# Kernel optimization log

Measured on AMD Instinct MI355X. Metric: run time of the kernel, lower is better.

The kernel has to match this reference:

```python
import jax, jax.numpy as jnp
import numpy as np

B, T, S, H, L = 64, 512, 400, 768, 9


def setup_inputs() -> dict:
    rng = np.random.default_rng(0)
    attn = np.zeros((B, T), np.int32)
    ids_lens = np.zeros((B, S), np.int32)
    for bi in range(B):
        Lb = int(rng.integers(T // 2, T + 1))  # valid wordpiece count
        lens = []
        rem = Lb
        while rem > 0 and len(lens) < S - 1:
            l = int(min(rng.integers(1, 4), rem))  # 1-3 wordpieces per word
            lens.append(l)
            rem -= l
        if rem > 0:
            lens.append(rem)
        attn[bi, :Lb] = 1
        ids_lens[bi, :len(lens)] = np.asarray(lens, np.int32)
    label_ids = rng.integers(0, L, (B, S)).astype(np.int32)
    label_mask = ids_lens > 0
    key = jax.random.key(0)
    k1, k2 = jax.random.split(key)
    last_enc_out = jax.random.normal(k1, (B, T, H), jnp.float32)
    W = jax.random.normal(k2, (H, L), jnp.float32) * 0.02
    b = jnp.zeros((L,), jnp.float32)
    return {
        'last_enc_out': last_enc_out, 'W': W, 'b': b,
        'attention_mask': jnp.asarray(attn), 'ids_lens': jnp.asarray(ids_lens),
        'label_ids': jnp.asarray(label_ids), 'label_mask': jnp.asarray(label_mask),
    }


def reference(last_enc_out, W, b, attention_mask, ids_lens, label_ids, label_mask):
    Bv, Tv, Hv = last_enc_out.shape
    Sv = ids_lens.shape[1]
    # position of each valid token among the row's valid tokens
    tok_pos = jnp.cumsum(attention_mask, axis=1) - 1            # [B,T]
    cum = jnp.cumsum(ids_lens, axis=1)                          # [B,S] nondecreasing
    # word index for each token: first w with cum[w] > tok_pos
    word_idx = jax.vmap(lambda c, p: jnp.searchsorted(c, p, side='right'))(cum, tok_pos)
    valid = attention_mask > 0
    seg = jnp.where(valid, jnp.arange(Bv)[:, None] * Sv + word_idx, Bv * Sv)  # dump slot for pad
    sums = jax.ops.segment_sum(last_enc_out.reshape(Bv * Tv, Hv), seg.reshape(Bv * Tv),
                               num_segments=Bv * Sv + 1)[:Bv * Sv]
    counts = jnp.maximum(ids_lens.reshape(Bv * Sv), 1).astype(last_enc_out.dtype)
    means = (sums / counts[:, None]).reshape(Bv, Sv, Hv)
    word_mask = ids_lens > 0
    bert_embed = jnp.where(word_mask[:, :, None], means, jnp.zeros((), last_enc_out.dtype))
    # dropout is identity in eval mode
    logits = bert_embed @ W + b                                 # [B,S,L]
    logp = jax.nn.log_softmax(logits, axis=-1)
    nll = -jnp.take_along_axis(logp, label_ids[..., None].astype(jnp.int32), axis=-1)[..., 0]
    mf = label_mask.astype(logits.dtype)
    loss = jnp.sum(nll * mf) / jnp.sum(mf)                      # CE with ignore_index masking
    output = jnp.argmax(logits, axis=-1)
    return loss, output
```

## Files before the change

### kernel.cpp

```cpp
#include <hip/hip_runtime.h>
#include <math.h>

#define Bdim 64
#define Tdim 512
#define Sdim 400
#define Hdim 768
#define Ldim 9

#define QWIN 130
#define LPROJ_ROWS 132

template <int CTRL>
__device__ __forceinline__ float dpp_add(float x) {
  int y = __builtin_amdgcn_update_dpp(0, __float_as_int(x), CTRL, 0xF, 0xF, false);
  return x + __int_as_float(y);
}
__device__ __forceinline__ float wave_sum63(float x) {
  x = dpp_add<0x111>(x);
  x = dpp_add<0x112>(x);
  x = dpp_add<0x114>(x);
  x = dpp_add<0x118>(x);
  x = dpp_add<0x142>(x);
  x = dpp_add<0x143>(x);
  return x;
}

__global__ __launch_bounds__(512, 2) void fused_kernel(
    const float* __restrict__ enc, const float* __restrict__ W,
    const float* __restrict__ bias, const int* __restrict__ attn,
    const int* __restrict__ ids_lens, const int* __restrict__ label_ids,
    float* __restrict__ out, float2* __restrict__ partials) {
  int blk = blockIdx.x;
  int b = blk >> 2;
  int part = blk & 3;
  int q0 = part << 7;
  int tid = threadIdx.x;
  int lane = tid & 63, wid = tid >> 6;

  __shared__ int p2t[Tdim];
  __shared__ int wst[Sdim];
  __shared__ float lproj[LPROJ_ROWS][12];
  __shared__ int wsum[8];
  __shared__ int totsm;
  __shared__ float ssm[8], csm[8];

  int m = attn[b * Tdim + tid];
  int x = m;
#pragma unroll
  for (int off = 1; off < 64; off <<= 1) {
    int v = __shfl_up(x, off, 64);
    if (lane >= off) x += v;
  }
  if (lane == 63) wsum[wid] = x;
  __syncthreads();
  if (tid < 8) {
    int s = wsum[tid], y = s;
#pragma unroll
    for (int off = 1; off < 8; off <<= 1) {
      int v = __shfl_up(y, off, 64);
      if (tid >= off) y += v;
    }
    wsum[tid] = y - s;
    if (tid == 7) totsm = y;
  }
  __syncthreads();
  x += wsum[wid];
  if (m) p2t[x - 1] = tid;
  int nv = totsm;
  __syncthreads();

  int len = (tid < Sdim) ? ids_lens[b * Sdim + tid] : 0;
  int x2 = len;
#pragma unroll
  for (int off = 1; off < 64; off <<= 1) {
    int v = __shfl_up(x2, off, 64);
    if (lane >= off) x2 += v;
  }
  if (lane == 63) wsum[wid] = x2;
  __syncthreads();
  if (tid < 8) {
    int s = wsum[tid], y = s;
#pragma unroll
    for (int off = 1; off < 8; off <<= 1) {
      int v = __shfl_up(y, off, 64);
      if (tid >= off) y += v;
    }
    wsum[tid] = y - s;
  }
  __syncthreads();
  x2 += wsum[wid];
  if (tid < Sdim) wst[tid] = x2 - len;
  __syncthreads();

  int lim = q0 + QWIN;
  if (lim > nv) lim = nv;
  if (wid < 6) {
    int g = (wid >= 3) ? 1 : 0;
    int l0 = (wid - 3 * g) * 3;
    int tc = lim - q0 - g;
    tc = (tc > 0) ? ((tc + 1) >> 1) : 0;

    if (tc > 0) {
      float wf[3][4][3];
#pragma unroll
      for (int k = 0; k < 3; ++k)
#pragma unroll
        for (int j = 0; j < 4; ++j) {
          int h = 4 * lane + 256 * k + j;
#pragma unroll
          for (int c = 0; c < 3; ++c) wf[k][j][c] = W[(size_t)h * Ldim + l0 + c];
        }
      const float4* encb = (const float4*)enc + (size_t)(b << 9) * (Hdim / 4);

      float4 A0, A1, A2, B0, B1, B2;
#define LDK(V0, V1, V2, K)                                                 \
  {                                                                        \
    int t_ = p2t[q0 + g + 2 * (K)];                                        \
    const float4* r_ = encb + (size_t)t_ * (Hdim / 4);                     \
    V0 = r_[lane]; V1 = r_[lane + 64]; V2 = r_[lane + 128];                \
  }
#define PRK(V0, V1, V2, K)                                                 \
  {                                                                        \
    float dd[3];                                                           \
    _Pragma("unroll") for (int c = 0; c < 3; ++c) {                        \
      dd[c] = V0.x * wf[0][0][c] + V0.y * wf[0][1][c] +                    \
              V0.z * wf[0][2][c] + V0.w * wf[0][3][c] +                    \
              V1.x * wf[1][0][c] + V1.y * wf[1][1][c] +                    \
              V1.z * wf[1][2][c] + V1.w * wf[1][3][c] +                    \
              V2.x * wf[2][0][c] + V2.y * wf[2][1][c] +                    \
              V2.z * wf[2][2][c] + V2.w * wf[2][3][c];                     \
      dd[c] = wave_sum63(dd[c]);                                           \
    }                                                                      \
    if (lane == 63) {                                                      \
      int row_ = g + 2 * (K);                                              \
      lproj[row_][l0 + 0] = dd[0];                                         \
      lproj[row_][l0 + 1] = dd[1];                                         \
      lproj[row_][l0 + 2] = dd[2];                                         \
    }                                                                      \
  }
      LDK(A0, A1, A2, 0)
      if (tc > 1) LDK(B0, B1, B2, 1)
      int k = 0;
      for (; k + 2 < tc; k += 2) {
        PRK(A0, A1, A2, k)
        LDK(A0, A1, A2, k + 2)
        PRK(B0, B1, B2, k + 1)
        if (k + 3 < tc) LDK(B0, B1, B2, k + 3)
      }
      PRK(A0, A1, A2, k)
      if (k + 1 < tc) PRK(B0, B1, B2, k + 1)
#undef LDK
#undef PRK
    }
  }
  __syncthreads();

  float nll = 0.0f, cnt = 0.0f;
  if (tid < Sdim) {
    int st = wst[tid];
    int stc = (st > 511) ? 511 : st;
    if ((stc >> 7) == part) {
      int bs = b * Sdim + tid;
      float sum[Ldim];
#pragma unroll
      for (int l = 0; l < Ldim; ++l) sum[l] = 0.0f;
      if (len > 0) {
        for (int j = 0; j < len; ++j) {
          int q = st + j;
          if (q >= nv) break;
          const float* pr = lproj[q - q0];
#pragma unroll
          for (int l = 0; l < Ldim; ++l) sum[l] += pr[l];
        }
      }
      float inv = (len > 0) ? 1.0f / (float)len : 0.0f;
      float lg[Ldim];
#pragma unroll
      for (int l = 0; l < Ldim; ++l) lg[l] = sum[l] * inv + bias[l];

      int amax = 0;
      float mx = lg[0];
#pragma unroll
      for (int l = 1; l < Ldim; ++l)
        if (lg[l] > mx) { mx = lg[l]; amax = l; }
      out[1 + bs] = (float)amax;

      if (len > 0) {
        float se = 0.0f;
#pragma unroll
        for (int l = 0; l < Ldim; ++l) se += expf(lg[l] - mx);
        float lse = mx + logf(se);
        int lab = label_ids[bs];
        float ll = lg[0];
#pragma unroll
        for (int l = 1; l < Ldim; ++l) ll = (lab == l) ? lg[l] : ll;
        nll = lse - ll;
        cnt = 1.0f;
      }
    }
  }

#pragma unroll
  for (int off = 32; off > 0; off >>= 1) {
    nll += __shfl_down(nll, off, 64);
    cnt += __shfl_down(cnt, off, 64);
  }
  if (lane == 0) { ssm[wid] = nll; csm[wid] = cnt; }
  __syncthreads();
  if (tid == 0) {
    float S = 0.f, C = 0.f;
#pragma unroll
    for (int k = 0; k < 8; ++k) { S += ssm[k]; C += csm[k]; }
    float2 pc; pc.x = S; pc.y = C;
    partials[blk] = pc;
  }
}

__global__ __launch_bounds__(256) void final_kernel(
    const float2* __restrict__ partials, float* __restrict__ out) {
  int tid = threadIdx.x;
  float2 pc = partials[tid];
  float s = pc.x, c = pc.y;
#pragma unroll
  for (int off = 32; off > 0; off >>= 1) {
    s += __shfl_down(s, off, 64);
    c += __shfl_down(c, off, 64);
  }
  __shared__ float ss[4], cc[4];
  int wid = tid >> 6, lane = tid & 63;
  if (lane == 0) { ss[wid] = s; cc[wid] = c; }
  __syncthreads();
  if (tid == 0)
    out[0] = (ss[0] + ss[1] + ss[2] + ss[3]) / (cc[0] + cc[1] + cc[2] + cc[3]);
}

extern "C" void kernel_launch(void* const* d_in, const int* in_sizes, int n_in,
                              void* d_out, int out_size, void* d_ws, size_t ws_size,
                              hipStream_t stream) {
  const float* enc     = (const float*)d_in[0];
  const float* W       = (const float*)d_in[1];
  const float* bias    = (const float*)d_in[2];
  const int* attn      = (const int*)d_in[3];
  const int* ids_lens  = (const int*)d_in[4];
  const int* label_ids = (const int*)d_in[5];

  float* out = (float*)d_out;

  float2* partials = (float2*)d_ws;

  fused_kernel<<<Bdim * 4, 512, 0, stream>>>(enc, W, bias, attn, ids_lens,
                                             label_ids, out, partials);
  final_kernel<<<1, 256, 0, stream>>>(partials, out);
}
```

Before: 33.00 us.

## Use all 8 waves for projection with all 9 labels each; fuse final reduction via atomics

New measurement: 36.40 us. +10.3%, slower.

```diff
diff --git a/kernel.cpp b/kernel.cpp
--- a/kernel.cpp
+++ b/kernel.cpp
@@ -25,11 +25,12 @@
   return x;
 }
 
-__global__ __launch_bounds__(512, 2) void fused_kernel(
+__global__ __launch_bounds__(512, 1) void fused_kernel(
     const float* __restrict__ enc, const float* __restrict__ W,
     const float* __restrict__ bias, const int* __restrict__ attn,
     const int* __restrict__ ids_lens, const int* __restrict__ label_ids,
-    float* __restrict__ out, float2* __restrict__ partials) {
+    float* __restrict__ out, float* __restrict__ accum,
+    unsigned* __restrict__ counter) {
   int blk = blockIdx.x;
   int b = blk >> 2;
   int part = blk & 3;
@@ -92,50 +93,46 @@
   if (tid < Sdim) wst[tid] = x2 - len;
   __syncthreads();
 
-  int lim = q0 + QWIN;
-  if (lim > nv) lim = nv;
-  if (wid < 6) {
-    int g = (wid >= 3) ? 1 : 0;
-    int l0 = (wid - 3 * g) * 3;
-    int tc = lim - q0 - g;
-    tc = (tc > 0) ? ((tc + 1) >> 1) : 0;
+  {
+    int lim = q0 + QWIN;
+    if (lim > nv) lim = nv;
+    int tc = lim - q0 - wid;
+    tc = (tc > 0) ? ((tc + 7) >> 3) : 0;
 
     if (tc > 0) {
-      float wf[3][4][3];
-#pragma unroll
-      for (int k = 0; k < 3; ++k)
+      float wf[3][4][Ldim];
+#pragma unroll
+      for (int c = 0; c < 3; ++c)
 #pragma unroll
         for (int j = 0; j < 4; ++j) {
-          int h = 4 * lane + 256 * k + j;
-#pragma unroll
-          for (int c = 0; c < 3; ++c) wf[k][j][c] = W[(size_t)h * Ldim + l0 + c];
+          int h = 4 * lane + 256 * c + j;
+#pragma unroll
+          for (int l = 0; l < Ldim; ++l) wf[c][j][l] = W[(size_t)h * Ldim + l];
         }
       const float4* encb = (const float4*)enc + (size_t)(b << 9) * (Hdim / 4);
 
       float4 A0, A1, A2, B0, B1, B2;
 #define LDK(V0, V1, V2, K)                                                 \
   {                                                                        \
-    int t_ = p2t[q0 + g + 2 * (K)];                                        \
+    int t_ = p2t[q0 + wid + 8 * (K)];                                      \
     const float4* r_ = encb + (size_t)t_ * (Hdim / 4);                     \
     V0 = r_[lane]; V1 = r_[lane + 64]; V2 = r_[lane + 128];                \
   }
 #define PRK(V0, V1, V2, K)                                                 \
   {                                                                        \
-    float dd[3];                                                           \
-    _Pragma("unroll") for (int c = 0; c < 3; ++c) {                        \
-      dd[c] = V0.x * wf[0][0][c] + V0.y * wf[0][1][c] +                    \
-              V0.z * wf[0][2][c] + V0.w * wf[0][3][c] +                    \
-              V1.x * wf[1][0][c] + V1.y * wf[1][1][c] +                    \
-              V1.z * wf[1][2][c] + V1.w * wf[1][3][c] +                    \
-              V2.x * wf[2][0][c] + V2.y * wf[2][1][c] +                    \
-              V2.z * wf[2][2][c] + V2.w * wf[2][3][c];                     \
-      dd[c] = wave_sum63(dd[c]);                                           \
+    float dd[Ldim];                                                        \
+    _Pragma("unroll") for (int l = 0; l < Ldim; ++l) {                     \
+      dd[l] = V0.x * wf[0][0][l] + V0.y * wf[0][1][l] +                    \
+              V0.z * wf[0][2][l] + V0.w * wf[0][3][l] +                    \
+              V1.x * wf[1][0][l] + V1.y * wf[1][1][l] +                    \
+              V1.z * wf[1][2][l] + V1.w * wf[1][3][l] +                    \
+              V2.x * wf[2][0][l] + V2.y * wf[2][1][l] +                    \
+              V2.z * wf[2][2][l] + V2.w * wf[2][3][l];                     \
+      dd[l] = wave_sum63(dd[l]);                                           \
     }                                                                      \
     if (lane == 63) {                                                      \
-      int row_ = g + 2 * (K);                                              \
-      lproj[row_][l0 + 0] = dd[0];                                         \
-      lproj[row_][l0 + 1] = dd[1];                                         \
-      lproj[row_][l0 + 2] = dd[2];                                         \
+      float* dst = lproj[wid + 8 * (K)];                                   \
+      _Pragma("unroll") for (int l = 0; l < Ldim; ++l) dst[l] = dd[l];     \
     }                                                                      \
   }
       LDK(A0, A1, A2, 0)
@@ -211,27 +208,24 @@
     float S = 0.f, C = 0.f;
 #pragma unroll
     for (int k = 0; k < 8; ++k) { S += ssm[k]; C += csm[k]; }
-    float2 pc; pc.x = S; pc.y = C;
-    partials[blk] = pc;
-  }
-}
-
-__global__ __launch_bounds__(256) void final_kernel(
-    const float2* __restrict__ partials, float* __restrict__ out) {
-  int tid = threadIdx.x;
-  float2 pc = partials[tid];
-  float s = pc.x, c = pc.y;
-#pragma unroll
-  for (int off = 32; off > 0; off >>= 1) {
-    s += __shfl_down(s, off, 64);
-    c += __shfl_down(c, off, 64);
-  }
-  __shared__ float ss[4], cc[4];
-  int wid = tid >> 6, lane = tid & 63;
-  if (lane == 0) { ss[wid] = s; cc[wid] = c; }
-  __syncthreads();
-  if (tid == 0)
-    out[0] = (ss[0] + ss[1] + ss[2] + ss[3]) / (cc[0] + cc[1] + cc[2] + cc[3]);
+    atomicAdd(&accum[0], S);
+    atomicAdd(&accum[1], C);
+    __threadfence();
+    unsigned prev = atomicAdd(counter, 1u);
+    if (prev == gridDim.x - 1) {
+      __threadfence();
+      float Sf = atomicAdd(&accum[0], 0.0f);
+      float Cf = atomicAdd(&accum[1], 0.0f);
+      out[0] = Sf / Cf;
+    }
+  }
+}
+
+__global__ void init_kernel(float* __restrict__ accum,
+                            unsigned* __restrict__ counter) {
+  accum[0] = 0.0f;
+  accum[1] = 0.0f;
+  *counter = 0u;
 }
 
 extern "C" void kernel_launch(void* const* d_in, const int* in_sizes, int n_in,
@@ -246,9 +240,11 @@
 
   float* out = (float*)d_out;
 
-  float2* partials = (float2*)d_ws;
-
+  char* ws = (char*)d_ws;
+  float* accum      = (float*)ws;
+  unsigned* counter = (unsigned*)(ws + 128);
+
+  init_kernel<<<1, 1, 0, stream>>>(accum, counter);
   fused_kernel<<<Bdim * 4, 512, 0, stream>>>(enc, W, bias, attn, ids_lens,
-                                             label_ids, out, partials);
-  final_kernel<<<1, 256, 0, stream>>>(partials, out);
-}
+                                             label_ids, out, accum, counter);
+}
```
